# Performance work log

Hardware: AMD Instinct MI355X
Metric: run time of the kernel (lower is better)

The kernel has to match this reference:

```python
import jax, jax.numpy as jnp
import numpy as np

B, M, N, DQ, H = 4, 4096, 4096, 256, 64

def setup_inputs() -> dict:
    key = jax.random.key(0)
    k1, k2, k3, k4 = jax.random.split(key, 4)
    x = jax.random.normal(k1, (B, M, DQ), dtype=jnp.float32)
    cond = jax.random.normal(k2, (B, N, DQ), dtype=jnp.float32)
    Wq = jax.random.normal(k3, (DQ, H), dtype=jnp.float32) * (1.0 / np.sqrt(DQ))
    Wkv = jax.random.normal(k4, (DQ, 2 * H), dtype=jnp.float32) * (1.0 / np.sqrt(DQ))
    return {"x": x, "cond": cond, "Wq": Wq, "Wkv": Wkv}

def reference(x, cond, Wq, Wkv):
    h = Wq.shape[1]
    q = jnp.einsum('bmi,ih->bmh', x, Wq)          # [B,M,H]
    kv = jnp.einsum('bni,ih->bnh', cond, Wkv)     # [B,N,2H]
    k, v = jnp.split(kv, 2, axis=-1)              # each [B,N,H]
    qk = jnp.einsum('bmd,bnd->bmn', q, k) / jnp.sqrt(jnp.asarray(h, q.dtype))
    attn = jax.nn.softmax(qk, axis=-1)            # [B,M,N]
    out = jnp.einsum('bmn,bnd->bmd', attn, v)     # [B,M,H]
    return out
```

## Files before the change

kernel.cpp:

```cpp
#include <hip/hip_runtime.h>
#include <hip/hip_bf16.h>
#include <cstdint>


#define BB 4
#define MM 4096
#define NN 4096
#define DQm 256
#define DH 64
#define NSP 8
#define NITER (NN / 64 / NSP)
#define QSCALE 0.18033688011112042f

typedef _Float16 half8 __attribute__((ext_vector_type(8)));
typedef _Float16 half4 __attribute__((ext_vector_type(4)));
typedef float floatx16 __attribute__((ext_vector_type(16)));

static __device__ __forceinline__ unsigned pkrtz(float a, float b) {
    union { __fp16 h __attribute__((ext_vector_type(2))); unsigned u; } cv;
    cv.h = __builtin_amdgcn_cvt_pkrtz(a, b);
    return cv.u;
}

static __device__ __forceinline__ void gload16(const void* g, void* l) {
    __builtin_amdgcn_global_load_lds(
        (const __attribute__((address_space(1))) void*)g,
        (__attribute__((address_space(3))) void*)l, 16, 0, 0);
}

__global__ __launch_bounds__(256) void wtrans_kernel(const float* __restrict__ Wq,
                                                     const float* __restrict__ Wkv,
                                                     _Float16* __restrict__ wt) {
    int cout = blockIdx.x;
    int t = threadIdx.x;
    float v = (cout < 64) ? Wq[t * 64 + cout] * QSCALE : Wkv[t * 128 + (cout - 64)];
    _Float16 hi = (_Float16)v;
    _Float16 lo = (_Float16)(v - (float)hi);
    wt[cout * DQm + t] = hi;
    wt[192 * DQm + cout * DQm + t] = lo;
}

__global__ __launch_bounds__(256) void proj_kernel(const float* __restrict__ x,
                                                   const float* __restrict__ cond,
                                                   const _Float16* __restrict__ wt,
                                                   _Float16* __restrict__ q_h,
                                                   _Float16* __restrict__ k_h,
                                                   _Float16* __restrict__ vt_h) {
    __shared__ __align__(16) _Float16 xh[32][264];
    __shared__ __align__(16) _Float16 xl[32][264];
    const int t = threadIdx.x;
    const bool isq = blockIdx.x < (BB * MM / 32);
    const int blk = isq ? blockIdx.x : blockIdx.x - BB * MM / 32;
    const long row0 = (long)blk * 32;
    const float4* xg = (const float4*)((isq ? x : cond) + row0 * DQm);
#pragma unroll
    for (int it = 0; it < 8; ++it) {
        int fid = t + it * 256;
        int row = fid >> 6, c4 = fid & 63;
        float4 v = xg[fid];
        half4 hh = {(_Float16)v.x, (_Float16)v.y, (_Float16)v.z, (_Float16)v.w};
        half4 hl = {(_Float16)(v.x - (float)hh[0]), (_Float16)(v.y - (float)hh[1]),
                    (_Float16)(v.z - (float)hh[2]), (_Float16)(v.w - (float)hh[3])};
        *(half4*)(&xh[row][c4 * 4]) = hh;
        *(half4*)(&xl[row][c4 * 4]) = hl;
    }
    __syncthreads();
    const int lane = t & 63, w = t >> 6, c = lane & 31, h = lane >> 5;
    const _Float16* wlo = wt + 192 * DQm;

    if (isq) {
        const int kh = w & 1, ct = w >> 1;
        floatx16 a1, a2, a3;
#pragma unroll
        for (int i = 0; i < 16; ++i) { a1[i] = 0.f; a2[i] = 0.f; a3[i] = 0.f; }
#pragma unroll
        for (int k8 = 0; k8 < 8; ++k8) {
            int kt = kh * 8 + k8;
            half8 ah = *(const half8*)(&xh[c][kt * 16 + h * 8]);
            half8 al = *(const half8*)(&xl[c][kt * 16 + h * 8]);
            half8 bh = *(const half8*)(wt  + (long)(ct * 32 + c) * DQm + kt * 16 + h * 8);
            half8 bl = *(const half8*)(wlo + (long)(ct * 32 + c) * DQm + kt * 16 + h * 8);
            a1 = __builtin_amdgcn_mfma_f32_32x32x16_f16(ah, bh, a1, 0, 0, 0);
            a2 = __builtin_amdgcn_mfma_f32_32x32x16_f16(ah, bl, a2, 0, 0, 0);
            a3 = __builtin_amdgcn_mfma_f32_32x32x16_f16(al, bh, a3, 0, 0, 0);
        }
        float s[16];
#pragma unroll
        for (int i = 0; i < 16; ++i) s[i] = a1[i] + a2[i] + a3[i];
        float* red = (float*)&xh[0][0];
        __syncthreads();
        if (kh == 1) {
#pragma unroll
            for (int i = 0; i < 16; ++i) red[ct * 1024 + i * 64 + lane] = s[i];
        }
        __syncthreads();
        if (kh == 0) {
#pragma unroll
            for (int i = 0; i < 16; ++i) s[i] += red[ct * 1024 + i * 64 + lane];
#pragma unroll
            for (int r = 0; r < 16; ++r) {
                int m = (r & 3) + 8 * (r >> 2) + 4 * h;
                q_h[(row0 + m) * DH + ct * 32 + c] = (_Float16)s[r];
            }
        }
    } else {
        const int ct = w;
        floatx16 a1, a2, a3;
#pragma unroll
        for (int i = 0; i < 16; ++i) { a1[i] = 0.f; a2[i] = 0.f; a3[i] = 0.f; }
        const long wrow = 64 + ct * 32 + c;
#pragma unroll
        for (int kt = 0; kt < 16; ++kt) {
            half8 ah = *(const half8*)(&xh[c][kt * 16 + h * 8]);
            half8 al = *(const half8*)(&xl[c][kt * 16 + h * 8]);
            half8 bh = *(const half8*)(wt  + wrow * DQm + kt * 16 + h * 8);
            half8 bl = *(const half8*)(wlo + wrow * DQm + kt * 16 + h * 8);
            a1 = __builtin_amdgcn_mfma_f32_32x32x16_f16(ah, bh, a1, 0, 0, 0);
            a2 = __builtin_amdgcn_mfma_f32_32x32x16_f16(ah, bl, a2, 0, 0, 0);
            a3 = __builtin_amdgcn_mfma_f32_32x32x16_f16(al, bh, a3, 0, 0, 0);
        }
        int cout = ct * 32 + c;
        if (cout < 64) {
#pragma unroll
            for (int r = 0; r < 16; ++r) {
                int m = (r & 3) + 8 * (r >> 2) + 4 * h;
                k_h[(row0 + m) * DH + cout] = (_Float16)(a1[r] + a2[r] + a3[r]);
            }
        } else {
            int d = cout - 64;
            long bb = row0 >> 12;
#pragma unroll
            for (int s2 = 0; s2 < 4; ++s2) {
                long n = row0 + 8 * s2 + 4 * h;
                half4 hv;
#pragma unroll
                for (int j = 0; j < 4; ++j)
                    hv[j] = (_Float16)(a1[s2 * 4 + j] + a2[s2 * 4 + j] +
                                       a3[s2 * 4 + j]);
                *(half4*)(vt_h + (bb * DH + d) * NN + (n & 4095)) = hv;
            }
        }
    }
}

__global__ __launch_bounds__(256, 4) void fa_kernel(const _Float16* __restrict__ q_h,
                                                    const _Float16* __restrict__ k_h,
                                                    const _Float16* __restrict__ vt_h,
                                                    _Float16* __restrict__ Opart,
                                                    float2* __restrict__ ml) {
    __shared__ __align__(16) _Float16 k_lds[2][64][64];
    __shared__ __align__(16) _Float16 vt_lds[2][64][64];

    const int t = threadIdx.x;
    const int w = t >> 6;
    const int lane = t & 63;
    const int c = lane & 31;
    const int h = lane >> 5;

    const int bid = blockIdx.x;
    const int sp = bid >> 7;
    const int b  = (bid >> 5) & 3;
    const int mt = bid & 31;
    const int mbase = mt * 128 + w * 32;
    const long qrow = (long)b * MM + mbase + c;

    const int p0 = w * 2048 + (lane << 4);
    const int p1 = p0 + 1024;
    const int q0 = p0 ^ (((p0 >> 7) & 7) << 4);
    const int q1 = p1 ^ (((p1 >> 7) & 7) << 4);
    const int n0f = sp * NITER * 64;
    const char* ks0 = (const char*)k_h + ((long)b * NN + n0f) * DH * 2 + q0;
    const char* ks1 = (const char*)k_h + ((long)b * NN + n0f) * DH * 2 + q1;
    const char* vs0 = (const char*)vt_h +
                      (((long)b * DH + (p0 >> 7)) * NN + n0f) * 2 + (q0 & 127);
    const char* vs1 = (const char*)vt_h +
                      (((long)b * DH + (p1 >> 7)) * NN + n0f) * 2 + (q1 & 127);

#define STAGE(bufi)                                                   \
    do {                                                              \
        char* kld = (char*)(&k_lds[bufi][0][0]) + w * 2048;           \
        char* vld = (char*)(&vt_lds[bufi][0][0]) + w * 2048;          \
        gload16(ks0, kld);                                            \
        gload16(ks1, kld + 1024);                                     \
        gload16(vs0, vld);                                            \
        gload16(vs1, vld + 1024);                                     \
        ks0 += 64 * DH * 2; ks1 += 64 * DH * 2;                       \
        vs0 += 128; vs1 += 128;                                       \
    } while (0)

    const int swb = (c & 7) << 4;
    int koff[4];
#pragma unroll
    for (int kt = 0; kt < 4; ++kt) koff[kt] = (kt * 32 + h * 16) ^ swb;

    half8 qf[4];
#pragma unroll
    for (int kt = 0; kt < 4; ++kt)
        qf[kt] = *(const half8*)(q_h + qrow * DH + kt * 16 + h * 8);

    floatx16 Oc0, Oc1;
#pragma unroll
    for (int i = 0; i < 16; ++i) { Oc0[i] = 0.f; Oc1[i] = 0.f; }
    float l4[4] = {0.f, 0.f, 0.f, 0.f};
    float m_run = 8.0f;

    STAGE(0);
    __syncthreads();

#pragma unroll 1
    for (int it = 0; it < NITER; ++it) {
        const int pb = it & 1;
        if (it + 1 < NITER) STAGE(pb ^ 1);

        const char* kbase = (const char*)(&k_lds[pb][0][0]);
        const char* vbase = (const char*)(&vt_lds[pb][0][0]);

        floatx16 Sc[2];
        const float negm = -m_run;
        __builtin_amdgcn_s_setprio(1);
#pragma unroll
        for (int a = 0; a < 2; ++a) {
            floatx16 acc;
#pragma unroll
            for (int i = 0; i < 16; ++i) acc[i] = negm;
#pragma unroll
            for (int kt = 0; kt < 4; ++kt) {
                half8 af = *(const half8*)(kbase + (a * 32 + c) * 128 + koff[kt]);
                acc = __builtin_amdgcn_mfma_f32_32x32x16_f16(af, qf[kt], acc, 0, 0, 0);
            }
            Sc[a] = acc;
        }
        __builtin_amdgcn_s_setprio(0);

        float t3[11];
#pragma unroll
        for (int i = 0; i < 10; ++i) {
            float u0 = (3 * i < 16) ? Sc[0][3 * i] : Sc[1][3 * i - 16];
            float u1 = (3 * i + 1 < 16) ? Sc[0][3 * i + 1] : Sc[1][3 * i - 15];
            float u2 = (3 * i + 2 < 16) ? Sc[0][3 * i + 2] : Sc[1][3 * i - 14];
            t3[i] = fmaxf(fmaxf(u0, u1), u2);
        }
        t3[10] = fmaxf(Sc[1][14], Sc[1][15]);
        float m0 = fmaxf(fmaxf(t3[0], t3[1]), t3[2]);
        float m1 = fmaxf(fmaxf(t3[3], t3[4]), t3[5]);
        float m2 = fmaxf(fmaxf(t3[6], t3[7]), t3[8]);
        float lmax = fmaxf(fmaxf(m0, m1), fmaxf(m2, fmaxf(t3[9], t3[10])));
        if (__any(lmax > 8.0f)) {
            float tt = fmaxf(lmax, __shfl_xor(lmax, 32, 64));
            float alpha = exp2f(-tt);
#pragma unroll
            for (int j = 0; j < 4; ++j) l4[j] *= alpha;
#pragma unroll
            for (int i = 0; i < 16; ++i) { Oc0[i] *= alpha; Oc1[i] *= alpha; }
#pragma unroll
            for (int a = 0; a < 2; ++a)
#pragma unroll
                for (int r = 0; r < 16; ++r) Sc[a][r] -= tt;
            m_run += tt;
        }
#pragma unroll
        for (int a = 0; a < 2; ++a)
#pragma unroll
            for (int r = 0; r < 16; ++r) Sc[a][r] = exp2f(Sc[a][r]);

#pragma unroll
        for (int a = 0; a < 2; ++a) {
            uint2 pk0 = {pkrtz(Sc[a][0],  Sc[a][1]),  pkrtz(Sc[a][2],  Sc[a][3])};
            uint2 pk1 = {pkrtz(Sc[a][4],  Sc[a][5]),  pkrtz(Sc[a][6],  Sc[a][7])};
            uint2 pk2 = {pkrtz(Sc[a][8],  Sc[a][9]),  pkrtz(Sc[a][10], Sc[a][11])};
            uint2 pk3 = {pkrtz(Sc[a][12], Sc[a][13]), pkrtz(Sc[a][14], Sc[a][15])};
            union { uint4 u; half8 f; } f0, f1;
#if __has_builtin(__builtin_amdgcn_permlane32_swap)
            {
                auto r0s = __builtin_amdgcn_permlane32_swap(pk0.x, pk1.x, false, false);
                auto r1s = __builtin_amdgcn_permlane32_swap(pk0.y, pk1.y, false, false);
                auto r2s = __builtin_amdgcn_permlane32_swap(pk2.x, pk3.x, false, false);
                auto r3s = __builtin_amdgcn_permlane32_swap(pk2.y, pk3.y, false, false);
                f0.u.x = r0s[0]; f0.u.z = r0s[1];
                f0.u.y = r1s[0]; f0.u.w = r1s[1];
                f1.u.x = r2s[0]; f1.u.z = r2s[1];
                f1.u.y = r3s[0]; f1.u.w = r3s[1];
            }
#else
            {
                uint2 s0, s1, ex0, ex1;
                s0.x = h ? pk0.x : pk1.x;  s0.y = h ? pk0.y : pk1.y;
                s1.x = h ? pk2.x : pk3.x;  s1.y = h ? pk2.y : pk3.y;
                ex0.x = __shfl_xor((int)s0.x, 32, 64);
                ex0.y = __shfl_xor((int)s0.y, 32, 64);
                ex1.x = __shfl_xor((int)s1.x, 32, 64);
                ex1.y = __shfl_xor((int)s1.y, 32, 64);
                f0.u.x = h ? ex0.x : pk0.x;  f0.u.y = h ? ex0.y : pk0.y;
                f0.u.z = h ? pk1.x : ex0.x;  f0.u.w = h ? pk1.y : ex0.y;
                f1.u.x = h ? ex1.x : pk2.x;  f1.u.y = h ? ex1.y : pk2.y;
                f1.u.z = h ? pk3.x : ex1.x;  f1.u.w = h ? pk3.y : ex1.y;
            }
#endif
            __builtin_amdgcn_s_setprio(1);
#pragma unroll
            for (int bq = 0; bq < 2; ++bq) {
                int kt = 2 * a + bq;
                half8 pf = bq ? f1.f : f0.f;
                half8 vf0 = *(const half8*)(vbase + c * 128 + koff[kt]);
                half8 vf1 = *(const half8*)(vbase + (32 + c) * 128 + koff[kt]);
                Oc0 = __builtin_amdgcn_mfma_f32_32x32x16_f16(vf0, pf, Oc0, 0, 0, 0);
                Oc1 = __builtin_amdgcn_mfma_f32_32x32x16_f16(vf1, pf, Oc1, 0, 0, 0);
            }
            __builtin_amdgcn_s_setprio(0);
        }

        {
            float t16v[8];
#pragma unroll
            for (int i = 0; i < 8; ++i)
                t16v[i] = (Sc[0][i] + Sc[0][i + 8]) + (Sc[1][i] + Sc[1][i + 8]);
#pragma unroll
            for (int j = 0; j < 4; ++j) l4[j] += t16v[j] + t16v[j + 4];
        }

        __syncthreads();
    }
#undef STAGE

    float lsum = (l4[0] + l4[1]) + (l4[2] + l4[3]);
    lsum += __shfl_xor(lsum, 32, 64);
    const float inv = 1.0f / lsum;
    const long obase = ((long)sp * BB * MM + (long)b * MM + mbase + c) * DH;
#pragma unroll
    for (int dt = 0; dt < 2; ++dt) {
        const floatx16& O = dt ? Oc1 : Oc0;
#pragma unroll
        for (int s2 = 0; s2 < 4; ++s2) {
            uint2 hv;
            hv.x = pkrtz(O[s2 * 4 + 0] * inv, O[s2 * 4 + 1] * inv);
            hv.y = pkrtz(O[s2 * 4 + 2] * inv, O[s2 * 4 + 3] * inv);
            *(uint2*)(Opart + obase + dt * 32 + s2 * 8 + h * 4) = hv;
        }
    }
    if (h == 0)
        ml[((long)sp * BB + b) * MM + mbase + c] = make_float2(m_run, lsum);
}

__global__ __launch_bounds__(256) void merge_kernel(const _Float16* __restrict__ Opart,
                                                    const float2* __restrict__ ml,
                                                    float* __restrict__ out) {
    const long g8 = (long)blockIdx.x * 256 + threadIdx.x;
    const long row = g8 >> 3;
    float2 p[NSP];
    float mmax = -INFINITY;
#pragma unroll
    for (int i = 0; i < NSP; ++i) {
        p[i] = ml[(long)i * BB * MM + row];
        mmax = fmaxf(mmax, p[i].x);
    }
    float denom = 0.f;
    float o[8] = {0.f, 0.f, 0.f, 0.f, 0.f, 0.f, 0.f, 0.f};
#pragma unroll
    for (int i = 0; i < NSP; ++i) {
        float wi = exp2f(p[i].x - mmax) * p[i].y;
        denom += wi;
        half8 v = *(const half8*)(Opart + (long)i * (BB * MM * DH) + g8 * 8);
#pragma unroll
        for (int j = 0; j < 8; ++j) o[j] += wi * (float)v[j];
    }
    float inv = 1.0f / denom;
    float4 o0 = {o[0] * inv, o[1] * inv, o[2] * inv, o[3] * inv};
    float4 o1 = {o[4] * inv, o[5] * inv, o[6] * inv, o[7] * inv};
    ((float4*)out)[g8 * 2] = o0;
    ((float4*)out)[g8 * 2 + 1] = o1;
}

extern "C" void kernel_launch(void* const* d_in, const int* in_sizes, int n_in,
                              void* d_out, int out_size, void* d_ws, size_t ws_size,
                              hipStream_t stream) {
    const float* x    = (const float*)d_in[0];
    const float* cond = (const float*)d_in[1];
    const float* Wq   = (const float*)d_in[2];
    const float* Wkv  = (const float*)d_in[3];
    float* out = (float*)d_out;

    char* ws = (char*)d_ws;
    _Float16* wt   = (_Float16*)(ws);
    _Float16* q_h  = (_Float16*)(ws + 196608);
    _Float16* k_h  = (_Float16*)(ws + 196608 + 2097152);
    _Float16* vt_h = (_Float16*)(ws + 196608 + 2 * 2097152);
    _Float16* Op   = (_Float16*)(ws + 196608 + 3 * 2097152);
    float2*   mlp  = (float2*)(ws + 196608 + 3 * 2097152 + (size_t)NSP * 2097152);

    wtrans_kernel<<<192, 256, 0, stream>>>(Wq, Wkv, wt);
    proj_kernel<<<BB * (MM + NN) / 32, 256, 0, stream>>>(x, cond, wt, q_h, k_h, vt_h);
    fa_kernel<<<NSP * BB * 32, 256, 0, stream>>>(q_h, k_h, vt_h, Op, mlp);
    merge_kernel<<<BB * MM * DH / 8 / 256, 256, 0, stream>>>(Op, mlp, out);
}
```

Before: 128.4 us.

## Fuse split-KV merge into attention kernel via last-block atomic counter

```diff
diff --git a/kernel.cpp b/kernel.cpp
--- a/kernel.cpp
+++ b/kernel.cpp
@@ -30,9 +30,11 @@
 
 __global__ __launch_bounds__(256) void wtrans_kernel(const float* __restrict__ Wq,
                                                      const float* __restrict__ Wkv,
-                                                     _Float16* __restrict__ wt) {
+                                                     _Float16* __restrict__ wt,
+                                                     unsigned* __restrict__ cnt) {
     int cout = blockIdx.x;
     int t = threadIdx.x;
+    if (cout == 0 && t < BB * 32) cnt[t] = 0;
     float v = (cout < 64) ? Wq[t * 64 + cout] * QSCALE : Wkv[t * 128 + (cout - 64)];
     _Float16 hi = (_Float16)v;
     _Float16 lo = (_Float16)(v - (float)hi);
@@ -147,7 +149,9 @@
                                                     const _Float16* __restrict__ k_h,
                                                     const _Float16* __restrict__ vt_h,
                                                     _Float16* __restrict__ Opart,
-                                                    float2* __restrict__ ml) {
+                                                    float2* __restrict__ ml,
+                                                    unsigned* __restrict__ cnt,
+                                                    float* __restrict__ out) {
     __shared__ __align__(16) _Float16 k_lds[2][64][64];
     __shared__ __align__(16) _Float16 vt_lds[2][64][64];
 
@@ -339,35 +343,44 @@
     }
     if (h == 0)
         ml[((long)sp * BB + b) * MM + mbase + c] = make_float2(m_run, lsum);
-}
-
-__global__ __launch_bounds__(256) void merge_kernel(const _Float16* __restrict__ Opart,
-                                                    const float2* __restrict__ ml,
-                                                    float* __restrict__ out) {
-    const long g8 = (long)blockIdx.x * 256 + threadIdx.x;
-    const long row = g8 >> 3;
-    float2 p[NSP];
-    float mmax = -INFINITY;
-#pragma unroll
-    for (int i = 0; i < NSP; ++i) {
-        p[i] = ml[(long)i * BB * MM + row];
-        mmax = fmaxf(mmax, p[i].x);
+
+    __threadfence();
+    __shared__ unsigned last;
+    if (t == 0) last = atomicAdd(&cnt[b * 32 + mt], 1u);
+    __syncthreads();
+    if (last == NSP - 1) {
+        __threadfence();
+        const long rowbase = (long)mt * 128;
+#pragma unroll
+        for (int cc = 0; cc < 4; ++cc) {
+            int chunk = t + cc * 256;
+            int row_l = chunk >> 3;
+            long row = rowbase + row_l;
+            float2 p[NSP];
+            float mmax = -INFINITY;
+#pragma unroll
+            for (int i = 0; i < NSP; ++i) {
+                p[i] = ml[((long)i * BB + b) * MM + row];
+                mmax = fmaxf(mmax, p[i].x);
+            }
+            float denom = 0.f;
+            float o[8] = {0.f, 0.f, 0.f, 0.f, 0.f, 0.f, 0.f, 0.f};
+            long g8 = ((long)b * MM + row) * 8 + (chunk & 7);
+#pragma unroll
+            for (int i = 0; i < NSP; ++i) {
+                float wi = exp2f(p[i].x - mmax) * p[i].y;
+                denom += wi;
+                half8 v = *(const half8*)(Opart + (long)i * (BB * MM * DH) + g8 * 8);
+#pragma unroll
+                for (int j = 0; j < 8; ++j) o[j] += wi * (float)v[j];
+            }
+            float invd = 1.0f / denom;
+            float4 o0 = {o[0] * invd, o[1] * invd, o[2] * invd, o[3] * invd};
+            float4 o1 = {o[4] * invd, o[5] * invd, o[6] * invd, o[7] * invd};
+            ((float4*)out)[g8 * 2] = o0;
+            ((float4*)out)[g8 * 2 + 1] = o1;
+        }
     }
-    float denom = 0.f;
-    float o[8] = {0.f, 0.f, 0.f, 0.f, 0.f, 0.f, 0.f, 0.f};
-#pragma unroll
-    for (int i = 0; i < NSP; ++i) {
-        float wi = exp2f(p[i].x - mmax) * p[i].y;
-        denom += wi;
-        half8 v = *(const half8*)(Opart + (long)i * (BB * MM * DH) + g8 * 8);
-#pragma unroll
-        for (int j = 0; j < 8; ++j) o[j] += wi * (float)v[j];
-    }
-    float inv = 1.0f / denom;
-    float4 o0 = {o[0] * inv, o[1] * inv, o[2] * inv, o[3] * inv};
-    float4 o1 = {o[4] * inv, o[5] * inv, o[6] * inv, o[7] * inv};
-    ((float4*)out)[g8 * 2] = o0;
-    ((float4*)out)[g8 * 2 + 1] = o1;
 }
 
 extern "C" void kernel_launch(void* const* d_in, const int* in_sizes, int n_in,
@@ -386,9 +399,10 @@
     _Float16* vt_h = (_Float16*)(ws + 196608 + 2 * 2097152);
     _Float16* Op   = (_Float16*)(ws + 196608 + 3 * 2097152);
     float2*   mlp  = (float2*)(ws + 196608 + 3 * 2097152 + (size_t)NSP * 2097152);
-
-    wtrans_kernel<<<192, 256, 0, stream>>>(Wq, Wkv, wt);
+    unsigned* cnt  = (unsigned*)(ws + 196608 + 3 * 2097152 +
+                                 (size_t)NSP * 2097152 + 1048576);
+
+    wtrans_kernel<<<192, 256, 0, stream>>>(Wq, Wkv, wt, cnt);
     proj_kernel<<<BB * (MM + NN) / 32, 256, 0, stream>>>(x, cond, wt, q_h, k_h, vt_h);
-    fa_kernel<<<NSP * BB * 32, 256, 0, stream>>>(q_h, k_h, vt_h, Op, mlp);
-    merge_kernel<<<BB * MM * DH / 8 / 256, 256, 0, stream>>>(Op, mlp, out);
-}
+    fa_kernel<<<NSP * BB * 32, 256, 0, stream>>>(q_h, k_h, vt_h, Op, mlp, cnt, out);
+}
```

After: 266.3 us. +107.4%, slower.
